# Kernel optimization log

Hardware: AMD Instinct MI355X
Metric: run time of the kernel (lower is better)

The kernel has to match this reference:

```python
import jax, jax.numpy as jnp
import numpy as np

OUTPUT_BIT = 8
N_SCALE = 28          # scale_bits
EXP_BITS = 16
SEGMENTS = 16
DEGREE = 2
S_VAL = 0.03          # input quantization scale


def _fit_pieces(s):
    # Mirrors _compute_integer_coefficients for backend='float':
    # fit exp((x_off-127)*s) over offset domain x_off*s in [-128s, 127s].
    xs_off = np.linspace(-128.0, 127.0, 10000)
    ys = np.exp((xs_off - 127.0) * s)
    xs = xs_off * s
    bounds = np.linspace(-128.0 * s, 127.0 * s, SEGMENTS + 1)
    coeffs = np.zeros((SEGMENTS, DEGREE + 1))  # ascending powers a0,a1,a2
    for j in range(SEGMENTS):
        m = (xs >= bounds[j]) & (xs <= bounds[j + 1])
        coeffs[j] = np.polyfit(xs[m], ys[m], DEGREE)[::-1]
    # integer coefficients: p(x_int*s)*2^N = sum_k floor(a_k*s^k*2^N)*x_int^k
    pw = s ** np.arange(DEGREE + 1)
    coeffs_int = np.floor(coeffs * pw[None, :] * (2.0 ** N_SCALE))
    lo_int = np.floor(bounds[:-1] / s)  # integer segment lower bounds
    return lo_int.astype(np.float32), coeffs_int.astype(np.float32)


def setup_inputs() -> dict:
    key = jax.random.key(0)
    x = jax.random.normal(key, (8, 12, 512, 512), dtype=jnp.float32) * 4.0
    scaling_factor = jnp.full((1,), S_VAL, dtype=jnp.float32)
    lo_np, cf_np = _fit_pieces(S_VAL)
    return {
        "x": x,
        "scaling_factor": scaling_factor,
        "lo_bounds": jnp.asarray(lo_np),
        "coeffs": jnp.asarray(cf_np),
    }


def floor_ste(y):
    # floor with straight-through gradient
    return y + jax.lax.stop_gradient(jnp.floor(y) - y)


def reference(x, scaling_factor, lo_bounds, coeffs):
    s = scaling_factor
    x_int = floor_ste(x / s)
    x_int = x_int - jnp.max(x_int, axis=-1, keepdims=True) + 127.0

    # piecewise-polynomial integer exp (computed under no_grad in the original)
    xi = jax.lax.stop_gradient(x_int)
    idx = jnp.clip(jnp.searchsorted(lo_bounds, xi, side="right") - 1, 0, SEGMENTS - 1)
    c = coeffs[idx]                         # [..., deg+1], ascending powers
    r = c[..., DEGREE]
    for k in range(DEGREE - 1, -1, -1):     # Horner evaluation
        r = r * xi + c[..., k]
    exp_int = jnp.maximum(jax.lax.stop_gradient(r), 0.0)

    exp_int = floor_ste(exp_int / 2.0 ** (30 - EXP_BITS + 1))
    exp_sum = jnp.maximum(jnp.sum(exp_int, axis=-1, keepdims=True), 1.0)
    factor = jnp.floor(2.0 ** 32 / jax.lax.stop_gradient(exp_sum))
    softmax_int = jnp.floor(jax.lax.stop_gradient(exp_int) * factor / 2.0 ** (32 - OUTPUT_BIT + 1))

    softmax_float = jax.nn.softmax(x, axis=-1)
    s_out = jnp.array([2.0 / 2 ** OUTPUT_BIT], dtype=x.dtype)
    smi_f = softmax_int * s_out
    # STE: integer value forward, float-softmax gradient backward
    output = jax.lax.stop_gradient(smi_f) + (softmax_float - jax.lax.stop_gradient(softmax_float))
    output = s_out * floor_ste(output / s_out)
    return output, s_out
```

## Files before the change

kernel.cpp:

```cpp
#include <hip/hip_runtime.h>


#define ROWLEN 512
#define ROWS_PER_WAVE 6

typedef float nfloat4 __attribute__((ext_vector_type(4)));

__global__ __launch_bounds__(256, 8) void ppis_kernel(
    const float* __restrict__ x,
    const float* __restrict__ sfp,
    const float* __restrict__ lo,
    const float* __restrict__ cf,
    float* __restrict__ out,
    int nrows)
{
    __shared__ int4 s_cf[16];

    const int tid  = threadIdx.x;
    const int lane = tid & 63;
    const int wid  = tid >> 6;

    if (tid < 16)
        s_cf[tid] = make_int4((int)cf[tid*3+0], (int)cf[tid*3+1], (int)cf[tid*3+2], 0);

    const float s  = sfp[0];
    const float ry = 1.0f / s;
    __syncthreads();

    const long long wgid = (long long)blockIdx.x * 4 + wid;
    const long long row0 = wgid * ROWS_PER_WAVE;

    const float4* xbase = reinterpret_cast<const float4*>(x);
    nfloat4*      obase = reinterpret_cast<nfloat4*>(out);

    float4 na, nb;
    {
        const float4* xp = xbase + row0 * (ROWLEN / 4);
        na = xp[lane];
        nb = xp[lane + 64];
    }

    #pragma unroll
    for (int r = 0; r < ROWS_PER_WAVE; ++r) {
        const long long row = row0 + r;
        const float4 va = na, vb = nb;
        if (r + 1 < ROWS_PER_WAVE) {
            const float4* xp = xbase + (row + 1) * (ROWLEN / 4);
            na = xp[lane];
            nb = xp[lane + 64];
        }

        const float xv[8] = {va.x, va.y, va.z, va.w, vb.x, vb.y, vb.z, vb.w};

        int n[8];
        #pragma unroll
        for (int k = 0; k < 8; ++k) {
            const float xk = xv[k];
            float nf = floorf(xk * ry);
            const float d = fmaf(-s, nf, xk);
            nf = (d < 0.0f) ? nf - 1.0f : nf;
            const float u = fmaf(-s, nf + 1.0f, xk);
            nf = (u >= 0.0f) ? nf + 1.0f : nf;
            n[k] = (int)nf;
        }

        int mx = max(max(max(n[0], n[1]), max(n[2], n[3])),
                     max(max(n[4], n[5]), max(n[6], n[7])));
        #pragma unroll
        for (int off = 32; off >= 1; off >>= 1)
            mx = max(mx, __shfl_xor(mx, off, 64));

        const int off255 = 255 - mx;

        int e[8];
        int tsum = 0;
        #pragma unroll
        for (int k = 0; k < 8; ++k) {
            const int u  = n[k] + off255;
            const int uc = u < 0 ? 0 : u;
            int idx = ((uc + 1) * 257) >> 12;
            idx = idx > 15 ? 15 : idx;
            const int4 c = s_cf[idx];
            const int xi = u - 128;
            const int r1 = c.z * xi + c.y;
            long long r2 = (long long)r1 * xi + c.x;
            if (r2 < 0) r2 = 0;
            e[k] = (int)(r2 >> 15);
            tsum += e[k];
        }

        #pragma unroll
        for (int off = 32; off >= 1; off >>= 1)
            tsum += __shfl_xor(tsum, off, 64);
        if (tsum < 1) tsum = 1;

        const unsigned int factor =
            (unsigned int)floor(__ddiv_rn(4294967296.0, (double)tsum));

        nfloat4 o0, o1;
        #pragma unroll
        for (int k = 0; k < 4; ++k) {
            const unsigned long long p0 = (unsigned long long)(unsigned int)e[k] * factor;
            const unsigned long long p1 = (unsigned long long)(unsigned int)e[k+4] * factor;
            o0[k] = (float)(int)(p0 >> 25) * 0.0078125f;
            o1[k] = (float)(int)(p1 >> 25) * 0.0078125f;
        }

        nfloat4* op = obase + row * (ROWLEN / 4);
        __builtin_nontemporal_store(o0, op + lane);
        __builtin_nontemporal_store(o1, op + lane + 64);
    }

    if (wgid == 0 && lane == 0)
        out[(long long)nrows * ROWLEN] = 0.0078125f;
}

extern "C" void kernel_launch(void* const* d_in, const int* in_sizes, int n_in,
                              void* d_out, int out_size, void* d_ws, size_t ws_size,
                              hipStream_t stream) {
    const float* x  = (const float*)d_in[0];
    const float* sf = (const float*)d_in[1];
    const float* lo = (const float*)d_in[2];
    const float* cf = (const float*)d_in[3];
    float* out = (float*)d_out;

    const int nrows = in_sizes[0] / ROWLEN;
    const int blocks = nrows / (ROWS_PER_WAVE * 4);
    ppis_kernel<<<blocks, 256, 0, stream>>>(x, sf, lo, cf, out, nrows);
}
```

Before: 190.9 us.

## Process one row per wave with DPP reductions and float-max before quantization

Each wave now handles a single row instead of six rows with software prefetch, so the grid is six times larger. The row max is taken on raw floats and then quantized once (floor-division is monotonic), and both the max and sum reductions use DPP row operations plus a readlane instead of shfl_xor butterflies. The aim is to cut reduction latency and per-element integer max work and to expose more parallelism. In exchange it drops the explicit next-row prefetch and pays per-block setup (coefficient load, syncthreads) six times as often.

```diff
diff --git a/kernel.cpp b/kernel.cpp
--- a/kernel.cpp
+++ b/kernel.cpp
@@ -2,9 +2,23 @@
 
 
 #define ROWLEN 512
-#define ROWS_PER_WAVE 6
 
 typedef float nfloat4 __attribute__((ext_vector_type(4)));
+
+#define DPP_SUM_I32(t)                                                        \
+    t += __builtin_amdgcn_update_dpp(0, t, 0x111, 0xf, 0xf, true);            \
+    t += __builtin_amdgcn_update_dpp(0, t, 0x112, 0xf, 0xf, true);            \
+    t += __builtin_amdgcn_update_dpp(0, t, 0x114, 0xf, 0xf, true);            \
+    t += __builtin_amdgcn_update_dpp(0, t, 0x118, 0xf, 0xf, true);            \
+    t += __builtin_amdgcn_update_dpp(0, t, 0x142, 0xa, 0xf, true);            \
+    t += __builtin_amdgcn_update_dpp(0, t, 0x143, 0xc, 0xf, true);
+
+#define DPP_MAX_F32_STEP(m, ctrl, rmask)                                      \
+    {                                                                         \
+        int _mi = __float_as_int(m);                                          \
+        int _sh = __builtin_amdgcn_update_dpp(_mi, _mi, ctrl, rmask, 0xf, false); \
+        m = fmaxf(m, __int_as_float(_sh));                                    \
+    }
 
 __global__ __launch_bounds__(256, 8) void ppis_kernel(
     const float* __restrict__ x,
@@ -27,91 +41,77 @@
     const float ry = 1.0f / s;
     __syncthreads();
 
-    const long long wgid = (long long)blockIdx.x * 4 + wid;
-    const long long row0 = wgid * ROWS_PER_WAVE;
+    const long long row = (long long)blockIdx.x * 4 + wid;
+    const float4* xp = reinterpret_cast<const float4*>(x) + row * (ROWLEN / 4);
+    const float4 va = xp[lane];
+    const float4 vb = xp[lane + 64];
 
-    const float4* xbase = reinterpret_cast<const float4*>(x);
-    nfloat4*      obase = reinterpret_cast<nfloat4*>(out);
+    const float xv[8] = {va.x, va.y, va.z, va.w, vb.x, vb.y, vb.z, vb.w};
 
-    float4 na, nb;
-    {
-        const float4* xp = xbase + row0 * (ROWLEN / 4);
-        na = xp[lane];
-        nb = xp[lane + 64];
+    float mf = fmaxf(fmaxf(fmaxf(xv[0], xv[1]), fmaxf(xv[2], xv[3])),
+                     fmaxf(fmaxf(xv[4], xv[5]), fmaxf(xv[6], xv[7])));
+    DPP_MAX_F32_STEP(mf, 0x111, 0xf)
+    DPP_MAX_F32_STEP(mf, 0x112, 0xf)
+    DPP_MAX_F32_STEP(mf, 0x114, 0xf)
+    DPP_MAX_F32_STEP(mf, 0x118, 0xf)
+    DPP_MAX_F32_STEP(mf, 0x142, 0xa)
+    DPP_MAX_F32_STEP(mf, 0x143, 0xc)
+    const float xmax = __int_as_float(__builtin_amdgcn_readlane(__float_as_int(mf), 63));
+
+    auto fdiv_floor = [&](float xk) -> int {
+        float nf = floorf(xk * ry);
+        const float d = fmaf(-s, nf, xk);
+        nf = (d < 0.0f) ? nf - 1.0f : nf;
+        const float u = fmaf(-s, nf + 1.0f, xk);
+        nf = (u >= 0.0f) ? nf + 1.0f : nf;
+        return (int)nf;
+    };
+
+    int n[8];
+    #pragma unroll
+    for (int k = 0; k < 8; ++k) n[k] = fdiv_floor(xv[k]);
+    const int mx = fdiv_floor(xmax);
+
+    const int off255 = 255 - mx;
+
+    int e[8];
+    int tsum = 0;
+    #pragma unroll
+    for (int k = 0; k < 8; ++k) {
+        const int u  = n[k] + off255;
+        const int uc = u < 0 ? 0 : u;
+        int idx = ((uc + 1) * 257) >> 12;
+        idx = idx > 15 ? 15 : idx;
+        const int4 c = s_cf[idx];
+        const int xi = u - 128;
+        const int r1 = c.z * xi + c.y;
+        long long r2 = (long long)r1 * xi + c.x;
+        if (r2 < 0) r2 = 0;
+        e[k] = (int)(r2 >> 15);
+        tsum += e[k];
     }
 
+    DPP_SUM_I32(tsum)
+    int ts = __builtin_amdgcn_readlane(tsum, 63);
+    if (ts < 1) ts = 1;
+
+    const unsigned int factor =
+        (unsigned int)floor(__ddiv_rn(4294967296.0, (double)ts));
+
+    nfloat4 o0, o1;
     #pragma unroll
-    for (int r = 0; r < ROWS_PER_WAVE; ++r) {
-        const long long row = row0 + r;
-        const float4 va = na, vb = nb;
-        if (r + 1 < ROWS_PER_WAVE) {
-            const float4* xp = xbase + (row + 1) * (ROWLEN / 4);
-            na = xp[lane];
-            nb = xp[lane + 64];
-        }
-
-        const float xv[8] = {va.x, va.y, va.z, va.w, vb.x, vb.y, vb.z, vb.w};
-
-        int n[8];
-        #pragma unroll
-        for (int k = 0; k < 8; ++k) {
-            const float xk = xv[k];
-            float nf = floorf(xk * ry);
-            const float d = fmaf(-s, nf, xk);
-            nf = (d < 0.0f) ? nf - 1.0f : nf;
-            const float u = fmaf(-s, nf + 1.0f, xk);
-            nf = (u >= 0.0f) ? nf + 1.0f : nf;
-            n[k] = (int)nf;
-        }
-
-        int mx = max(max(max(n[0], n[1]), max(n[2], n[3])),
-                     max(max(n[4], n[5]), max(n[6], n[7])));
-        #pragma unroll
-        for (int off = 32; off >= 1; off >>= 1)
-            mx = max(mx, __shfl_xor(mx, off, 64));
-
-        const int off255 = 255 - mx;
-
-        int e[8];
-        int tsum = 0;
-        #pragma unroll
-        for (int k = 0; k < 8; ++k) {
-            const int u  = n[k] + off255;
-            const int uc = u < 0 ? 0 : u;
-            int idx = ((uc + 1) * 257) >> 12;
-            idx = idx > 15 ? 15 : idx;
-            const int4 c = s_cf[idx];
-            const int xi = u - 128;
-            const int r1 = c.z * xi + c.y;
-            long long r2 = (long long)r1 * xi + c.x;
-            if (r2 < 0) r2 = 0;
-            e[k] = (int)(r2 >> 15);
-            tsum += e[k];
-        }
-
-        #pragma unroll
-        for (int off = 32; off >= 1; off >>= 1)
-            tsum += __shfl_xor(tsum, off, 64);
-        if (tsum < 1) tsum = 1;
-
-        const unsigned int factor =
-            (unsigned int)floor(__ddiv_rn(4294967296.0, (double)tsum));
-
-        nfloat4 o0, o1;
-        #pragma unroll
-        for (int k = 0; k < 4; ++k) {
-            const unsigned long long p0 = (unsigned long long)(unsigned int)e[k] * factor;
-            const unsigned long long p1 = (unsigned long long)(unsigned int)e[k+4] * factor;
-            o0[k] = (float)(int)(p0 >> 25) * 0.0078125f;
-            o1[k] = (float)(int)(p1 >> 25) * 0.0078125f;
-        }
-
-        nfloat4* op = obase + row * (ROWLEN / 4);
-        __builtin_nontemporal_store(o0, op + lane);
-        __builtin_nontemporal_store(o1, op + lane + 64);
+    for (int k = 0; k < 4; ++k) {
+        const unsigned long long p0 = (unsigned long long)(unsigned int)e[k]   * factor;
+        const unsigned long long p1 = (unsigned long long)(unsigned int)e[k+4] * factor;
+        o0[k] = (float)(int)(p0 >> 25) * 0.0078125f;
+        o1[k] = (float)(int)(p1 >> 25) * 0.0078125f;
     }
 
-    if (wgid == 0 && lane == 0)
+    nfloat4* op = reinterpret_cast<nfloat4*>(out) + row * (ROWLEN / 4);
+    __builtin_nontemporal_store(o0, op + lane);
+    __builtin_nontemporal_store(o1, op + lane + 64);
+
+    if (row == 0 && lane == 0)
         out[(long long)nrows * ROWLEN] = 0.0078125f;
 }
 
@@ -125,6 +125,5 @@
     float* out = (float*)d_out;
 
     const int nrows = in_sizes[0] / ROWLEN;
-    const int blocks = nrows / (ROWS_PER_WAVE * 4);
-    ppis_kernel<<<blocks, 256, 0, stream>>>(x, sf, lo, cf, out, nrows);
+    ppis_kernel<<<nrows / 4, 256, 0, stream>>>(x, sf, lo, cf, out, nrows);
 }
```

After: 183.6 us. -3.8%, faster.
